# Performance work log

Hardware: AMD Instinct MI355X
Metric: run time of the kernel (lower is better)

## Reference

```python
import jax, jax.numpy as jnp
import numpy as np

N = 30000          # nodes
DEG = 16           # in-degree per node
E = N * DEG        # edges per etype
T = 3              # edge types
IN = 128           # in_feats
HID = 256          # hidden_size
HEADS = 4
CLS = 2            # num_classes
NEG_SLOPE = 0.2    # DGL GATConv default


def setup_inputs() -> dict:
    key = jax.random.key(0)
    ks = jax.random.split(key, 14)
    s = lambda k, shape: (jax.random.normal(k, shape, jnp.float32) * 0.05)
    feat = jax.random.normal(ks[0], (N, IN), jnp.float32)
    src = jax.random.randint(ks[1], (T, E), 0, N)
    # every node gets exactly DEG incoming edges per etype (DGL forbids 0-in-degree)
    dst = jnp.tile(jnp.repeat(jnp.arange(N), DEG), (T, 1))
    D = HID // HEADS
    return {
        "feat": feat,
        "W0": s(ks[2], (T, IN, HID)),  "al0": s(ks[3], (T, HEADS, D)), "ar0": s(ks[4], (T, HEADS, D)), "b0": jnp.zeros((T, HID), jnp.float32),
        "W1": s(ks[5], (T, HID, HID)), "al1": s(ks[6], (T, HEADS, D)), "ar1": s(ks[7], (T, HEADS, D)), "b1": jnp.zeros((T, HID), jnp.float32),
        "W2": s(ks[8], (T, HID, CLS)), "al2": s(ks[9], (T, 1, CLS)),   "ar2": s(ks[10], (T, 1, CLS)), "b2": jnp.zeros((T, CLS), jnp.float32),
        "src": src, "dst": dst,
    }


def _gat(feat, W, al, ar, b, src, dst):
    """DGL GATConv: feat [n,F], W [F,H*D], al/ar [H,D], b [H*D] -> [n,H,D]."""
    n = feat.shape[0]
    H, D = al.shape
    h = (feat @ W).reshape(n, H, D)                      # projected features
    el = jnp.sum(h * al, axis=-1)                        # [n,H]
    er = jnp.sum(h * ar, axis=-1)                        # [n,H]
    e = jax.nn.leaky_relu(el[src] + er[dst], NEG_SLOPE)  # [E,H] edge scores
    # segment softmax over incoming edges of each dst node
    emax = jax.ops.segment_max(e, dst, num_segments=n)
    ex = jnp.exp(e - emax[dst])
    den = jax.ops.segment_sum(ex, dst, num_segments=n)
    alpha = ex / den[dst]                                # [E,H]
    out = jax.ops.segment_sum(h[src] * alpha[:, :, None], dst, num_segments=n)
    return out + b.reshape(H, D)


def _hetero(feat, W, al, ar, b, src, dst):
    # HeteroGraphConv(aggregate='mean') over T edge types on one node type
    outs = [_gat(feat, W[t], al[t], ar[t], b[t], src[t], dst[t]) for t in range(W.shape[0])]
    return jnp.mean(jnp.stack(outs, 0), axis=0)


def reference(feat, W0, al0, ar0, b0, W1, al1, ar1, b1, W2, al2, ar2, b2, src, dst):
    h = jax.nn.elu(_hetero(feat, W0, al0, ar0, b0, src, dst).reshape(N, -1))
    h = jax.nn.elu(_hetero(h, W1, al1, ar1, b1, src, dst).reshape(N, -1))
    logits = _hetero(h, W2, al2, ar2, b2, src, dst)      # [N,1,CLS]
    # faithful to F.softmax(logits[primary_ntype], dim=1): dim=1 is the size-1 head axis
    return logits, jax.nn.softmax(logits, axis=1)
```

## Files before the change

### kernel.cpp

```cpp
#include <hip/hip_runtime.h>
#include <hip/hip_bf16.h>
#include <hip/hip_fp8.h>
#include <math.h>

#define N_NODES 30000
#define DEG     16
#define NE      480000
#define NT      3
#define IN_F    128
#define HID_F   256
#define HEADS   4
#define DH      64
#define CLS     2
#define SLOPE   0.2f

#define NTILES      1875
#define KC0         4
#define KC1         8

typedef __hip_bfloat16 bf16;
typedef unsigned long long u64;
typedef __attribute__((ext_vector_type(8))) short short8;
typedef __attribute__((ext_vector_type(4))) float floatx4;

__device__ __forceinline__ float bf2f(short x) {
    unsigned int u = ((unsigned int)(unsigned short)x) << 16;
    float f;
    __builtin_memcpy(&f, &u, 4);
    return f;
}
__device__ __forceinline__ short f2bf_s(float x) {
    bf16 b = bf16(x);
    short s;
    __builtin_memcpy(&s, &b, 2);
    return s;
}

__device__ __forceinline__ void fp8x4_decode(unsigned int u, float* f) {
#if __has_builtin(__builtin_amdgcn_cvt_pk_f32_fp8)
    auto lo = __builtin_amdgcn_cvt_pk_f32_fp8((int)u, false);
    auto hi = __builtin_amdgcn_cvt_pk_f32_fp8((int)u, true);
    f[0] = lo[0]; f[1] = lo[1]; f[2] = hi[0]; f[3] = hi[1];
#else
#pragma unroll
    for (int j = 0; j < 4; j++) {
        __hip_fp8_e4m3 q;
        q.__x = (unsigned char)((u >> (8 * j)) & 0xff);
        f[j] = (float)q;
    }
#endif
}
__device__ __forceinline__ unsigned int fp8_encode4_u32(float v0, float v1,
                                                        float v2, float v3) {
#if __has_builtin(__builtin_amdgcn_cvt_pk_fp8_f32)
    int p01 = __builtin_amdgcn_cvt_pk_fp8_f32(v0, v1, 0, false);
    int p23 = __builtin_amdgcn_cvt_pk_fp8_f32(v2, v3, 0, false);
    return ((unsigned int)p01 & 0xffffu) | ((unsigned int)p23 << 16);
#else
    __hip_fp8_e4m3 q0(v0), q1(v1), q2(v2), q3(v3);
    return (unsigned int)q0.__x | ((unsigned int)q1.__x << 8) |
           ((unsigned int)q2.__x << 16) | ((unsigned int)q3.__x << 24);
#endif
}
__device__ __forceinline__ u64 fp8_encode8_u64(const float* v) {
    unsigned int lo = fp8_encode4_u32(v[0], v[1], v[2], v[3]);
    unsigned int hi = fp8_encode4_u32(v[4], v[5], v[6], v[7]);
    return (u64)lo | ((u64)hi << 32);
}


#define FEAT8_THREADS (N_NODES * (IN_F / 8))
#define BP0_THREADS   (NT * 16 * KC0 * 64)
#define BP1_THREADS   (NT * 16 * KC1 * 64)
__global__ void prep(const float* __restrict__ feat, const float* __restrict__ W0,
                     const float* __restrict__ W1, u64* __restrict__ feat8,
                     u64* __restrict__ Bpack0, u64* __restrict__ Bpack1) {
    int g = blockIdx.x * 256 + threadIdx.x;
    if (g < FEAT8_THREADS) {
        const float* src = feat + (size_t)g * 8;
        float v[8];
#pragma unroll
        for (int j = 0; j < 8; j++) v[j] = src[j];
        feat8[g] = fp8_encode8_u64(v);
        return;
    }
    g -= FEAT8_THREADS;
    if (g < BP0_THREADS) {
        int t = g / (16 * KC0 * 64), rem = g % (16 * KC0 * 64);
        int nt = rem / (KC0 * 64);
        int C  = (rem / 64) % KC0;
        int lane = rem & 63, l15 = lane & 15, quad = lane >> 4;
        int col = nt * 16 + l15, k0 = C * 32 + quad * 8;
        const float* src = W0 + (size_t)t * IN_F * HID_F + (size_t)k0 * HID_F + col;
        float v[8];
#pragma unroll
        for (int j = 0; j < 8; j++) v[j] = src[(size_t)j * HID_F];
        Bpack0[((size_t)(t * 16 + nt) * KC0 + C) * 64 + lane] = fp8_encode8_u64(v);
        return;
    }
    g -= BP0_THREADS;
    if (g < BP1_THREADS) {
        int t = g / (16 * KC1 * 64), rem = g % (16 * KC1 * 64);
        int nt = rem / (KC1 * 64);
        int C  = (rem / 64) % KC1;
        int lane = rem & 63, l15 = lane & 15, quad = lane >> 4;
        int col = nt * 16 + l15, k0 = C * 32 + quad * 8;
        const float* src = W1 + (size_t)t * HID_F * HID_F + (size_t)k0 * HID_F + col;
        float v[8];
#pragma unroll
        for (int j = 0; j < 8; j++) v[j] = src[(size_t)j * HID_F];
        Bpack1[((size_t)(t * 16 + nt) * KC1 + C) * 64 + lane] = fp8_encode8_u64(v);
    }
}

template <int K>
__global__ __launch_bounds__(256, 4) void gemm_proj(const unsigned char* __restrict__ X8,
                                                    const u64* __restrict__ Bpack,
                                                    const float* __restrict__ al,
                                                    const float* __restrict__ ar,
                                                    unsigned char* __restrict__ Hout,
                                                    float* __restrict__ el,
                                                    float* __restrict__ er) {
    const int KC = K / 32;
    __shared__ u64 sB[512 * (K / 32)];
    int nh   = blockIdx.y;
    int t    = blockIdx.z;
    int tid  = threadIdx.x;
    int wave = tid >> 6, lane = tid & 63;
    int quad = lane >> 4, l15 = lane & 15;
    int e0   = blockIdx.x * 8 + wave * 2;

    {
        const u64* Bp = Bpack + (size_t)(t * 16 + nh * 8) * KC * 64;
#pragma unroll
        for (int i = 0; i < 2 * KC; i++) sB[i * 256 + tid] = Bp[i * 256 + tid];
    }
    __syncthreads();

    int ra0 = e0 * 16 + l15;       if (ra0 >= N_NODES) ra0 = N_NODES - 1;
    int ra1 = (e0 + 1) * 16 + l15; if (ra1 >= N_NODES) ra1 = N_NODES - 1;
    const unsigned char* Ap0 = X8 + (size_t)ra0 * K + quad * 8;
    const unsigned char* Ap1 = X8 + (size_t)ra1 * K + quad * 8;
    unsigned char* Ht = Hout + (size_t)t * N_NODES * HID_F;

    floatx4 acc[8][2];
#pragma unroll
    for (int i = 0; i < 8; i++) {
        acc[i][0] = (floatx4){0.f, 0.f, 0.f, 0.f};
        acc[i][1] = (floatx4){0.f, 0.f, 0.f, 0.f};
    }

#pragma unroll
    for (int C = 0; C < KC; C++) {
        long xb0 = (long)*(const u64*)(Ap0 + C * 32);
        long xb1 = (long)*(const u64*)(Ap1 + C * 32);
#pragma unroll
        for (int nt = 0; nt < 8; nt++) {
            long wa = (long)sB[(nt * KC + C) * 64 + lane];
            acc[nt][0] = __builtin_amdgcn_mfma_f32_16x16x32_fp8_fp8(wa, xb0, acc[nt][0], 0, 0, 0);
            acc[nt][1] = __builtin_amdgcn_mfma_f32_16x16x32_fp8_fp8(wa, xb1, acc[nt][1], 0, 0, 0);
        }
    }

#pragma unroll
    for (int e = 0; e < 2; e++) {
        int node = (e0 + e) * 16 + l15;
        bool ok  = node < N_NODES;
#pragma unroll
        for (int nt = 0; nt < 8; nt++) {
            unsigned int u = fp8_encode4_u32(acc[nt][e][0], acc[nt][e][1],
                                             acc[nt][e][2], acc[nt][e][3]);
            if (ok)
                __builtin_nontemporal_store(u,
                    (unsigned int*)(Ht + (size_t)node * HID_F + (nh * 8 + nt) * 16 + quad * 4));
        }
#pragma unroll
        for (int hl = 0; hl < 2; hl++) {
            int h = nh * 2 + hl;
            float pl = 0.f, pr = 0.f;
#pragma unroll
            for (int j = 0; j < 4; j++) {
                int nt = hl * 4 + j;
                int coff = t * HID_F + (nh * 8 + nt) * 16 + quad * 4;
                float4 av = *(const float4*)(al + coff);
                float4 rv = *(const float4*)(ar + coff);
                pl += acc[nt][e][0] * av.x + acc[nt][e][1] * av.y +
                      acc[nt][e][2] * av.z + acc[nt][e][3] * av.w;
                pr += acc[nt][e][0] * rv.x + acc[nt][e][1] * rv.y +
                      acc[nt][e][2] * rv.z + acc[nt][e][3] * rv.w;
            }
            pl += __shfl_xor(pl, 16); pl += __shfl_xor(pl, 32);
            pr += __shfl_xor(pr, 16); pr += __shfl_xor(pr, 32);
            if (lane < 16 && ok) {
                el[((size_t)t * N_NODES + node) * HEADS + h] = pl;
                er[((size_t)t * N_NODES + node) * HEADS + h] = pr;
            }
        }
    }
}

template <bool PACK>
__global__ __launch_bounds__(256, 8) void gat_agg(const unsigned char* __restrict__ Hproj,
                                                  const float* __restrict__ el,
                                                  const float* __restrict__ er,
                                                  const int* __restrict__ src,
                                                  const float* __restrict__ bias,
                                                  void* __restrict__ outv) {
    int blk = blockIdx.x;
    int tid = threadIdx.x;
    __shared__ int   s_src[8][NT][DEG];
    __shared__ float s_w[8][NT][HEADS][DEG];

#pragma unroll
    for (int it = 0; it < 2; it++) {
        int j = it * 256 + tid;
        if (j < NT * 128) {
            int t = j / 128, k = j % 128;
            s_src[k >> 4][t][k & 15] = src[(size_t)t * NE + blk * 128 + k];
        }
    }
    __syncthreads();

    {
        int lane16 = tid & 15;
        int ubase  = tid >> 4;
#pragma unroll
        for (int it = 0; it < 6; it++) {
            int u = it * 16 + ubase;
            int g = u / 12, rem = u % 12;
            int t = rem >> 2, h = rem & 3;
            int n = blk * 8 + g;
            int s = s_src[g][t][lane16];
            float e = el[((size_t)t * N_NODES + s) * HEADS + h] +
                      er[((size_t)t * N_NODES + n) * HEADS + h];
            e = e > 0.f ? e : SLOPE * e;
            float m = e;
            m = fmaxf(m, __shfl_xor(m, 1));
            m = fmaxf(m, __shfl_xor(m, 2));
            m = fmaxf(m, __shfl_xor(m, 4));
            m = fmaxf(m, __shfl_xor(m, 8));
            float p = __expf(e - m);
            float ss = p;
            ss += __shfl_xor(ss, 1);
            ss += __shfl_xor(ss, 2);
            ss += __shfl_xor(ss, 4);
            ss += __shfl_xor(ss, 8);
            s_w[g][t][h][lane16] = p / ss;
        }
    }
    __syncthreads();

    int g = tid >> 5, c = tid & 31;
    int n = blk * 8 + g;
    int h = c >> 3;
    int col0 = c * 8;

    float acc[8];
#pragma unroll
    for (int j = 0; j < 8; j++) acc[j] = 0.f;

#pragma unroll
    for (int t = 0; t < NT; t++) {
        const unsigned char* Hh = Hproj + (size_t)t * N_NODES * HID_F;
#pragma unroll
        for (int i = 0; i < DEG; i++) {
            int s   = s_src[g][t][i];
            float w = s_w[g][t][h][i];
            uint2 v = *(const uint2*)(Hh + (size_t)s * HID_F + col0);
            float f[8];
            fp8x4_decode(v.x, f);
            fp8x4_decode(v.y, f + 4);
#pragma unroll
            for (int j = 0; j < 8; j++) acc[j] += w * f[j];
        }
    }

    float res[8];
#pragma unroll
    for (int j = 0; j < 8; j++) {
        float bsum = bias[0 * HID_F + col0 + j] + bias[1 * HID_F + col0 + j] +
                     bias[2 * HID_F + col0 + j];
        float r = (acc[j] + bsum) * (1.f / 3.f);
        res[j] = r > 0.f ? r : (__expf(r) - 1.f);
    }
    if (PACK) {
        u64* out = (u64*)outv;
        out[((size_t)n * HID_F + col0) >> 3] = fp8_encode8_u64(res);
    } else {
        short* out = (short*)outv;
        short8 o;
#pragma unroll
        for (int j = 0; j < 8; j++) o[j] = f2bf_s(res[j]);
        *(short8*)(out + (size_t)n * HID_F + col0) = o;
    }
}

__global__ __launch_bounds__(256) void proj2(const short* __restrict__ X,
                                             const float* __restrict__ W2,
                                             const float* __restrict__ al2,
                                             const float* __restrict__ ar2,
                                             float* __restrict__ p2,
                                             float* __restrict__ el2,
                                             float* __restrict__ er2) {
    int n    = blockIdx.x * 4 + (threadIdx.x >> 6);
    int lane = threadIdx.x & 63;
    const short* Xr = X + (size_t)n * HID_F + lane * 4;
    float x[4];
    x[0] = bf2f(Xr[0]); x[1] = bf2f(Xr[1]); x[2] = bf2f(Xr[2]); x[3] = bf2f(Xr[3]);
    float a[NT][CLS];
#pragma unroll
    for (int t = 0; t < NT; t++)
#pragma unroll
        for (int cc = 0; cc < CLS; cc++) {
            float v = 0.f;
#pragma unroll
            for (int j = 0; j < 4; j++)
                v += x[j] * W2[(size_t)t * HID_F * CLS + (lane * 4 + j) * CLS + cc];
#pragma unroll
            for (int off = 32; off; off >>= 1) v += __shfl_xor(v, off);
            a[t][cc] = v;
        }
    if (lane == 0) {
#pragma unroll
        for (int t = 0; t < NT; t++) {
            p2[((size_t)t * N_NODES + n) * CLS + 0] = a[t][0];
            p2[((size_t)t * N_NODES + n) * CLS + 1] = a[t][1];
            el2[(size_t)t * N_NODES + n] = a[t][0] * al2[t * CLS + 0] + a[t][1] * al2[t * CLS + 1];
            er2[(size_t)t * N_NODES + n] = a[t][0] * ar2[t * CLS + 0] + a[t][1] * ar2[t * CLS + 1];
        }
    }
}

__global__ void final_layer(const float* __restrict__ p2,
                            const float* __restrict__ el2,
                            const float* __restrict__ er2,
                            const int* __restrict__ src,
                            const float* __restrict__ b2,
                            float* __restrict__ out) {
    int n = blockIdx.x * 256 + threadIdx.x;
    if (n >= N_NODES) return;
    float l0 = 0.f, l1 = 0.f;
    for (int t = 0; t < NT; t++) {
        float erv = er2[(size_t)t * N_NODES + n];
        const int* sp = src + (size_t)t * NE + n * DEG;
        float ev[DEG];
        float m = -1e30f;
#pragma unroll
        for (int i = 0; i < DEG; i++) {
            int s   = sp[i];
            float e = el2[(size_t)t * N_NODES + s] + erv;
            e = e > 0.f ? e : SLOPE * e;
            ev[i] = e;
            m = fmaxf(m, e);
        }
        float den = 0.f, a0 = 0.f, a1 = 0.f;
#pragma unroll
        for (int i = 0; i < DEG; i++) {
            int s   = sp[i];
            float p = __expf(ev[i] - m);
            den += p;
            a0  += p * p2[((size_t)t * N_NODES + s) * CLS + 0];
            a1  += p * p2[((size_t)t * N_NODES + s) * CLS + 1];
        }
        l0 += a0 / den + b2[t * CLS + 0];
        l1 += a1 / den + b2[t * CLS + 1];
    }
    l0 *= (1.f / 3.f);
    l1 *= (1.f / 3.f);
    out[(size_t)n * CLS + 0] = l0;
    out[(size_t)n * CLS + 1] = l1;
    float* out2 = out + (size_t)N_NODES * CLS;
    out2[(size_t)n * CLS + 0] = 1.0f;
    out2[(size_t)n * CLS + 1] = 1.0f;
}

extern "C" void kernel_launch(void* const* d_in, const int* in_sizes, int n_in,
                              void* d_out, int out_size, void* d_ws, size_t ws_size,
                              hipStream_t stream) {
    const float* feat = (const float*)d_in[0];
    const float* W0   = (const float*)d_in[1];
    const float* al0  = (const float*)d_in[2];
    const float* ar0  = (const float*)d_in[3];
    const float* b0   = (const float*)d_in[4];
    const float* W1   = (const float*)d_in[5];
    const float* al1  = (const float*)d_in[6];
    const float* ar1  = (const float*)d_in[7];
    const float* b1   = (const float*)d_in[8];
    const float* W2   = (const float*)d_in[9];
    const float* al2  = (const float*)d_in[10];
    const float* ar2  = (const float*)d_in[11];
    const float* b2   = (const float*)d_in[12];
    const int*   src  = (const int*)d_in[13];

    char* w = (char*)d_ws;
    auto alloc = [&](size_t bytes) {
        char* p = w;
        w += (bytes + 255) & ~(size_t)255;
        return p;
    };
    u64* feat8  = (u64*)alloc((size_t)(N_NODES + 16) * IN_F);
    u64* h1_8   = (u64*)alloc((size_t)(N_NODES + 16) * HID_F);
    u64* Bpack0 = (u64*)alloc((size_t)NT * 16 * KC0 * 64 * 8);
    u64* Bpack1 = (u64*)alloc((size_t)NT * 16 * KC1 * 64 * 8);
    unsigned char* Hproj = (unsigned char*)alloc((size_t)NT * N_NODES * HID_F);
    short* h2    = (short*)alloc((size_t)N_NODES * HID_F * 2);
    float* el    = (float*)alloc((size_t)NT * N_NODES * HEADS * 4);
    float* er    = (float*)alloc((size_t)NT * N_NODES * HEADS * 4);
    float* p2    = (float*)alloc((size_t)NT * N_NODES * CLS * 4);
    float* el2   = (float*)alloc((size_t)NT * N_NODES * 4);
    float* er2   = (float*)alloc((size_t)NT * N_NODES * 4);

    int prep_total = FEAT8_THREADS + BP0_THREADS + BP1_THREADS;
    prep<<<(prep_total + 255) / 256, 256, 0, stream>>>(feat, W0, W1, feat8,
                                                       Bpack0, Bpack1);

    dim3 ggrid((NTILES + 7) / 8, 2, NT);

    gemm_proj<IN_F><<<ggrid, 256, 0, stream>>>((const unsigned char*)feat8, Bpack0,
                                               al0, ar0, Hproj, el, er);
    gat_agg<true><<<N_NODES / 8, 256, 0, stream>>>(Hproj, el, er, src, b0, h1_8);

    gemm_proj<HID_F><<<ggrid, 256, 0, stream>>>((const unsigned char*)h1_8, Bpack1,
                                                al1, ar1, Hproj, el, er);
    gat_agg<false><<<N_NODES / 8, 256, 0, stream>>>(Hproj, el, er, src, b1, h2);

    proj2<<<dim3(N_NODES / 4), 256, 0, stream>>>(h2, W2, al2, ar2, p2, el2, er2);
    final_layer<<<(N_NODES + 255) / 256, 256, 0, stream>>>(p2, el2, er2, src, b2,
                                                           (float*)d_out);
}
```

Measured before the change: 333.0 us.

## Aggregate raw features before projection and fold attention vectors into weights

```diff
diff --git a/kernel.cpp b/kernel.cpp
--- a/kernel.cpp
+++ b/kernel.cpp
@@ -14,26 +14,25 @@
 #define CLS     2
 #define SLOPE   0.2f
 
-#define NTILES      1875
-#define KC0         4
-#define KC1         8
+#define NBLK    1875
+#define KC0     4
+#define KC1     8
 
 typedef __hip_bfloat16 bf16;
 typedef unsigned long long u64;
-typedef __attribute__((ext_vector_type(8))) short short8;
 typedef __attribute__((ext_vector_type(4))) float floatx4;
 
+__device__ __forceinline__ short f2bf_s(float x) {
+    bf16 b = bf16(x);
+    short s;
+    __builtin_memcpy(&s, &b, 2);
+    return s;
+}
 __device__ __forceinline__ float bf2f(short x) {
     unsigned int u = ((unsigned int)(unsigned short)x) << 16;
     float f;
     __builtin_memcpy(&f, &u, 4);
     return f;
-}
-__device__ __forceinline__ short f2bf_s(float x) {
-    bf16 b = bf16(x);
-    short s;
-    __builtin_memcpy(&s, &b, 2);
-    return s;
 }
 
 __device__ __forceinline__ void fp8x4_decode(unsigned int u, float* f) {
@@ -68,13 +67,20 @@
     return (u64)lo | ((u64)hi << 32);
 }
 
-
 #define FEAT8_THREADS (N_NODES * (IN_F / 8))
 #define BP0_THREADS   (NT * 16 * KC0 * 64)
 #define BP1_THREADS   (NT * 16 * KC1 * 64)
-__global__ void prep(const float* __restrict__ feat, const float* __restrict__ W0,
-                     const float* __restrict__ W1, u64* __restrict__ feat8,
-                     u64* __restrict__ Bpack0, u64* __restrict__ Bpack1) {
+#define WL0_THREADS   (NT * HEADS * IN_F)
+#define WL1_THREADS   (NT * HEADS * HID_F)
+__global__ void prep(const float* __restrict__ feat,
+                     const float* __restrict__ W0, const float* __restrict__ al0,
+                     const float* __restrict__ ar0,
+                     const float* __restrict__ W1, const float* __restrict__ al1,
+                     const float* __restrict__ ar1,
+                     u64* __restrict__ feat8,
+                     u64* __restrict__ Bpack0, u64* __restrict__ Bpack1,
+                     float* __restrict__ wl0, float* __restrict__ wr0,
+                     float* __restrict__ wl1, float* __restrict__ wr1) {
     int g = blockIdx.x * 256 + threadIdx.x;
     if (g < FEAT8_THREADS) {
         const float* src = feat + (size_t)g * 8;
@@ -110,188 +116,218 @@
 #pragma unroll
         for (int j = 0; j < 8; j++) v[j] = src[(size_t)j * HID_F];
         Bpack1[((size_t)(t * 16 + nt) * KC1 + C) * 64 + lane] = fp8_encode8_u64(v);
+        return;
+    }
+    g -= BP1_THREADS;
+    if (g < WL0_THREADS) {
+        int u = g / IN_F, k = g % IN_F;
+        int t = u >> 2, h = u & 3;
+        const float* Wk = W0 + ((size_t)t * IN_F + k) * HID_F + h * DH;
+        const float* av = al0 + ((size_t)t * HEADS + h) * DH;
+        const float* rv = ar0 + ((size_t)t * HEADS + h) * DH;
+        float a = 0.f, b = 0.f;
+#pragma unroll 8
+        for (int d = 0; d < DH; d++) { float w = Wk[d]; a += w * av[d]; b += w * rv[d]; }
+        wl0[(size_t)u * IN_F + k] = a;
+        wr0[(size_t)u * IN_F + k] = b;
+        return;
+    }
+    g -= WL0_THREADS;
+    if (g < WL1_THREADS) {
+        int u = g / HID_F, k = g % HID_F;
+        int t = u >> 2, h = u & 3;
+        const float* Wk = W1 + ((size_t)t * HID_F + k) * HID_F + h * DH;
+        const float* av = al1 + ((size_t)t * HEADS + h) * DH;
+        const float* rv = ar1 + ((size_t)t * HEADS + h) * DH;
+        float a = 0.f, b = 0.f;
+#pragma unroll 8
+        for (int d = 0; d < DH; d++) { float w = Wk[d]; a += w * av[d]; b += w * rv[d]; }
+        wl1[(size_t)u * HID_F + k] = a;
+        wr1[(size_t)u * HID_F + k] = b;
     }
 }
 
 template <int K>
-__global__ __launch_bounds__(256, 4) void gemm_proj(const unsigned char* __restrict__ X8,
-                                                    const u64* __restrict__ Bpack,
-                                                    const float* __restrict__ al,
-                                                    const float* __restrict__ ar,
-                                                    unsigned char* __restrict__ Hout,
-                                                    float* __restrict__ el,
-                                                    float* __restrict__ er) {
+__global__ __launch_bounds__(256) void eler(const unsigned char* __restrict__ X8,
+                                            const float* __restrict__ wl,
+                                            const float* __restrict__ wr,
+                                            float* __restrict__ el,
+                                            float* __restrict__ er) {
+    const int KB = K / 64;
+    int n    = blockIdx.x * 4 + (threadIdx.x >> 6);
+    int lane = threadIdx.x & 63;
+    float f[KB > 4 ? KB : 4];
+    {
+        unsigned int u = 0;
+        if (KB == 2) {
+            unsigned short us;
+            __builtin_memcpy(&us, X8 + (size_t)n * K + lane * KB, 2);
+            u = us;
+        } else {
+            __builtin_memcpy(&u, X8 + (size_t)n * K + lane * KB, 4);
+        }
+        float d4[4];
+        fp8x4_decode(u, d4);
+#pragma unroll
+        for (int j = 0; j < KB; j++) f[j] = d4[j];
+    }
+#pragma unroll
+    for (int u = 0; u < NT * HEADS; u++) {
+        const float* wlv = wl + (size_t)u * K + lane * KB;
+        const float* wrv = wr + (size_t)u * K + lane * KB;
+        float a = 0.f, b = 0.f;
+#pragma unroll
+        for (int j = 0; j < KB; j++) { a += f[j] * wlv[j]; b += f[j] * wrv[j]; }
+#pragma unroll
+        for (int off = 32; off; off >>= 1) {
+            a += __shfl_xor(a, off);
+            b += __shfl_xor(b, off);
+        }
+        if (lane == 0) {
+            int t = u >> 2, h = u & 3;
+            el[((size_t)t * N_NODES + n) * HEADS + h] = a;
+            er[((size_t)t * N_NODES + n) * HEADS + h] = b;
+        }
+    }
+}
+
+template <int K, bool LAST>
+__global__ __launch_bounds__(256, 4) void fused_gat(
+    const unsigned char* __restrict__ X8,
+    const u64* __restrict__ Bpack,
+    const float* __restrict__ el,
+    const float* __restrict__ er,
+    const int* __restrict__ src,
+    const float* __restrict__ bias,
+    void* __restrict__ outv) {
     const int KC = K / 32;
-    __shared__ u64 sB[512 * (K / 32)];
-    int nh   = blockIdx.y;
-    int t    = blockIdx.z;
-    int tid  = threadIdx.x;
-    int wave = tid >> 6, lane = tid & 63;
-    int quad = lane >> 4, l15 = lane & 15;
-    int e0   = blockIdx.x * 8 + wave * 2;
-
-    {
-        const u64* Bp = Bpack + (size_t)(t * 16 + nh * 8) * KC * 64;
-#pragma unroll
-        for (int i = 0; i < 2 * KC; i++) sB[i * 256 + tid] = Bp[i * 256 + tid];
-    }
-    __syncthreads();
-
-    int ra0 = e0 * 16 + l15;       if (ra0 >= N_NODES) ra0 = N_NODES - 1;
-    int ra1 = (e0 + 1) * 16 + l15; if (ra1 >= N_NODES) ra1 = N_NODES - 1;
-    const unsigned char* Ap0 = X8 + (size_t)ra0 * K + quad * 8;
-    const unsigned char* Ap1 = X8 + (size_t)ra1 * K + quad * 8;
-    unsigned char* Ht = Hout + (size_t)t * N_NODES * HID_F;
-
-    floatx4 acc[8][2];
-#pragma unroll
-    for (int i = 0; i < 8; i++) {
-        acc[i][0] = (floatx4){0.f, 0.f, 0.f, 0.f};
-        acc[i][1] = (floatx4){0.f, 0.f, 0.f, 0.f};
-    }
-
-#pragma unroll
-    for (int C = 0; C < KC; C++) {
-        long xb0 = (long)*(const u64*)(Ap0 + C * 32);
-        long xb1 = (long)*(const u64*)(Ap1 + C * 32);
-#pragma unroll
-        for (int nt = 0; nt < 8; nt++) {
-            long wa = (long)sB[(nt * KC + C) * 64 + lane];
-            acc[nt][0] = __builtin_amdgcn_mfma_f32_16x16x32_fp8_fp8(wa, xb0, acc[nt][0], 0, 0, 0);
-            acc[nt][1] = __builtin_amdgcn_mfma_f32_16x16x32_fp8_fp8(wa, xb1, acc[nt][1], 0, 0, 0);
-        }
-    }
-
-#pragma unroll
-    for (int e = 0; e < 2; e++) {
-        int node = (e0 + e) * 16 + l15;
-        bool ok  = node < N_NODES;
-#pragma unroll
-        for (int nt = 0; nt < 8; nt++) {
-            unsigned int u = fp8_encode4_u32(acc[nt][e][0], acc[nt][e][1],
-                                             acc[nt][e][2], acc[nt][e][3]);
-            if (ok)
-                __builtin_nontemporal_store(u,
-                    (unsigned int*)(Ht + (size_t)node * HID_F + (nh * 8 + nt) * 16 + quad * 4));
-        }
-#pragma unroll
-        for (int hl = 0; hl < 2; hl++) {
-            int h = nh * 2 + hl;
-            float pl = 0.f, pr = 0.f;
-#pragma unroll
-            for (int j = 0; j < 4; j++) {
-                int nt = hl * 4 + j;
-                int coff = t * HID_F + (nh * 8 + nt) * 16 + quad * 4;
-                float4 av = *(const float4*)(al + coff);
-                float4 rv = *(const float4*)(ar + coff);
-                pl += acc[nt][e][0] * av.x + acc[nt][e][1] * av.y +
-                      acc[nt][e][2] * av.z + acc[nt][e][3] * av.w;
-                pr += acc[nt][e][0] * rv.x + acc[nt][e][1] * rv.y +
-                      acc[nt][e][2] * rv.z + acc[nt][e][3] * rv.w;
-            }
-            pl += __shfl_xor(pl, 16); pl += __shfl_xor(pl, 32);
-            pr += __shfl_xor(pr, 16); pr += __shfl_xor(pr, 32);
-            if (lane < 16 && ok) {
-                el[((size_t)t * N_NODES + node) * HEADS + h] = pl;
-                er[((size_t)t * N_NODES + node) * HEADS + h] = pr;
-            }
-        }
-    }
-}
-
-template <bool PACK>
-__global__ __launch_bounds__(256, 8) void gat_agg(const unsigned char* __restrict__ Hproj,
-                                                  const float* __restrict__ el,
-                                                  const float* __restrict__ er,
-                                                  const int* __restrict__ src,
-                                                  const float* __restrict__ bias,
-                                                  void* __restrict__ outv) {
+    const int KD = K / 128;
     int blk = blockIdx.x;
     int tid = threadIdx.x;
-    __shared__ int   s_src[8][NT][DEG];
-    __shared__ float s_w[8][NT][HEADS][DEG];
-
-#pragma unroll
-    for (int it = 0; it < 2; it++) {
-        int j = it * 256 + tid;
-        if (j < NT * 128) {
-            int t = j / 128, k = j % 128;
-            s_src[k >> 4][t][k & 15] = src[(size_t)t * NE + blk * 128 + k];
-        }
-    }
-    __syncthreads();
-
-    {
-        int lane16 = tid & 15;
-        int ubase  = tid >> 4;
-#pragma unroll
-        for (int it = 0; it < 6; it++) {
-            int u = it * 16 + ubase;
-            int g = u / 12, rem = u % 12;
-            int t = rem >> 2, h = rem & 3;
-            int n = blk * 8 + g;
-            int s = s_src[g][t][lane16];
-            float e = el[((size_t)t * N_NODES + s) * HEADS + h] +
-                      er[((size_t)t * N_NODES + n) * HEADS + h];
-            e = e > 0.f ? e : SLOPE * e;
-            float m = e;
-            m = fmaxf(m, __shfl_xor(m, 1));
-            m = fmaxf(m, __shfl_xor(m, 2));
-            m = fmaxf(m, __shfl_xor(m, 4));
-            m = fmaxf(m, __shfl_xor(m, 8));
-            float p = __expf(e - m);
-            float ss = p;
-            ss += __shfl_xor(ss, 1);
-            ss += __shfl_xor(ss, 2);
-            ss += __shfl_xor(ss, 4);
-            ss += __shfl_xor(ss, 8);
-            s_w[g][t][h][lane16] = p / ss;
-        }
-    }
-    __syncthreads();
-
-    int g = tid >> 5, c = tid & 31;
-    int n = blk * 8 + g;
-    int h = c >> 3;
-    int col0 = c * 8;
-
-    float acc[8];
-#pragma unroll
-    for (int j = 0; j < 8; j++) acc[j] = 0.f;
-
-#pragma unroll
+    int wave = tid >> 6, lane = tid & 63, quad = lane >> 4, l15 = lane & 15;
+
+    __shared__ int   s_src[256];
+    __shared__ float s_w[HEADS][16][17];
+    __shared__ u64   s_frag[HEADS][KC * 64];
+
+    floatx4 acc[HEADS];
+#pragma unroll
+    for (int h = 0; h < HEADS; h++) acc[h] = (floatx4){0.f, 0.f, 0.f, 0.f};
+
     for (int t = 0; t < NT; t++) {
-        const unsigned char* Hh = Hproj + (size_t)t * N_NODES * HID_F;
-#pragma unroll
-        for (int i = 0; i < DEG; i++) {
-            int s   = s_src[g][t][i];
-            float w = s_w[g][t][h][i];
-            uint2 v = *(const uint2*)(Hh + (size_t)s * HID_F + col0);
-            float f[8];
-            fp8x4_decode(v.x, f);
-            fp8x4_decode(v.y, f + 4);
-#pragma unroll
-            for (int j = 0; j < 8; j++) acc[j] += w * f[j];
-        }
-    }
-
-    float res[8];
-#pragma unroll
-    for (int j = 0; j < 8; j++) {
-        float bsum = bias[0 * HID_F + col0 + j] + bias[1 * HID_F + col0 + j] +
-                     bias[2 * HID_F + col0 + j];
-        float r = (acc[j] + bsum) * (1.f / 3.f);
-        res[j] = r > 0.f ? r : (__expf(r) - 1.f);
-    }
-    if (PACK) {
-        u64* out = (u64*)outv;
-        out[((size_t)n * HID_F + col0) >> 3] = fp8_encode8_u64(res);
-    } else {
-        short* out = (short*)outv;
-        short8 o;
-#pragma unroll
-        for (int j = 0; j < 8; j++) o[j] = f2bf_s(res[j]);
-        *(short8*)(out + (size_t)n * HID_F + col0) = o;
+        __syncthreads();
+        s_src[tid] = src[(size_t)t * NE + blk * 256 + tid];
+        __syncthreads();
+
+        {
+            int node = tid >> 4, i = tid & 15;
+            int s = s_src[node * 16 + i];
+            float4 eL = *(const float4*)(el + ((size_t)t * N_NODES + s) * HEADS);
+            float4 eR = *(const float4*)(er + ((size_t)t * N_NODES + blk * 16 + node) * HEADS);
+            float e0 = eL.x + eR.x, e1 = eL.y + eR.y, e2 = eL.z + eR.z, e3 = eL.w + eR.w;
+            e0 = e0 > 0.f ? e0 : SLOPE * e0;
+            e1 = e1 > 0.f ? e1 : SLOPE * e1;
+            e2 = e2 > 0.f ? e2 : SLOPE * e2;
+            e3 = e3 > 0.f ? e3 : SLOPE * e3;
+            float m0 = e0, m1 = e1, m2 = e2, m3 = e3;
+#pragma unroll
+            for (int off = 8; off; off >>= 1) {
+                m0 = fmaxf(m0, __shfl_xor(m0, off));
+                m1 = fmaxf(m1, __shfl_xor(m1, off));
+                m2 = fmaxf(m2, __shfl_xor(m2, off));
+                m3 = fmaxf(m3, __shfl_xor(m3, off));
+            }
+            float p0 = __expf(e0 - m0), p1 = __expf(e1 - m1);
+            float p2 = __expf(e2 - m2), p3 = __expf(e3 - m3);
+            float q0 = p0, q1 = p1, q2 = p2, q3 = p3;
+#pragma unroll
+            for (int off = 8; off; off >>= 1) {
+                q0 += __shfl_xor(q0, off);
+                q1 += __shfl_xor(q1, off);
+                q2 += __shfl_xor(q2, off);
+                q3 += __shfl_xor(q3, off);
+            }
+            s_w[0][node][i] = p0 / q0;
+            s_w[1][node][i] = p1 / q1;
+            s_w[2][node][i] = p2 / q2;
+            s_w[3][node][i] = p3 / q3;
+        }
+        __syncthreads();
+
+        {
+            int node = tid & 15, cg = tid >> 4;
+            const int* sp = s_src + node * 16;
+            float xacc[HEADS][8 * KD];
+#pragma unroll
+            for (int h = 0; h < HEADS; h++)
+#pragma unroll
+                for (int j = 0; j < 8 * KD; j++) xacc[h][j] = 0.f;
+
+#pragma unroll
+            for (int i = 0; i < DEG; i++) {
+                int s   = sp[i];
+                float w0 = s_w[0][node][i], w1 = s_w[1][node][i];
+                float w2 = s_w[2][node][i], w3 = s_w[3][node][i];
+#pragma unroll
+                for (int d = 0; d < KD; d++) {
+                    int c8 = cg + 16 * d;
+                    u64 v;
+                    __builtin_memcpy(&v, X8 + (size_t)s * K + c8 * 8, 8);
+                    float f[8];
+                    fp8x4_decode((unsigned int)v, f);
+                    fp8x4_decode((unsigned int)(v >> 32), f + 4);
+#pragma unroll
+                    for (int j = 0; j < 8; j++) {
+                        xacc[0][d * 8 + j] += w0 * f[j];
+                        xacc[1][d * 8 + j] += w1 * f[j];
+                        xacc[2][d * 8 + j] += w2 * f[j];
+                        xacc[3][d * 8 + j] += w3 * f[j];
+                    }
+                }
+            }
+#pragma unroll
+            for (int h = 0; h < HEADS; h++)
+#pragma unroll
+                for (int d = 0; d < KD; d++) {
+                    int c8 = cg + 16 * d, C = c8 >> 2, qf = c8 & 3;
+                    s_frag[h][C * 64 + qf * 16 + node] = fp8_encode8_u64(&xacc[h][d * 8]);
+                }
+        }
+        __syncthreads();
+
+        const u64* Bp = Bpack + (size_t)t * 16 * KC * 64;
+#pragma unroll
+        for (int h = 0; h < HEADS; h++) {
+#pragma unroll
+            for (int C = 0; C < KC; C++) {
+                long wa = (long)Bp[(size_t)((h * 4 + wave) * KC + C) * 64 + lane];
+                long xb = (long)s_frag[h][C * 64 + lane];
+                acc[h] = __builtin_amdgcn_mfma_f32_16x16x32_fp8_fp8(wa, xb, acc[h], 0, 0, 0);
+            }
+        }
+    }
+
+    int n = blk * 16 + l15;
+#pragma unroll
+    for (int h = 0; h < HEADS; h++) {
+        int col0 = h * 64 + wave * 16 + quad * 4;
+        float r[4];
+#pragma unroll
+        for (int j = 0; j < 4; j++) {
+            float bsum = bias[col0 + j] + bias[HID_F + col0 + j] + bias[2 * HID_F + col0 + j];
+            float v = (acc[h][j] + bsum) * (1.f / 3.f);
+            r[j] = v > 0.f ? v : (__expf(v) - 1.f);
+        }
+        if (LAST) {
+            u64 o = (u64)(unsigned short)f2bf_s(r[0]) |
+                    ((u64)(unsigned short)f2bf_s(r[1]) << 16) |
+                    ((u64)(unsigned short)f2bf_s(r[2]) << 32) |
+                    ((u64)(unsigned short)f2bf_s(r[3]) << 48);
+            *(u64*)((short*)outv + (size_t)n * HID_F + col0) = o;
+        } else {
+            unsigned int o = fp8_encode4_u32(r[0], r[1], r[2], r[3]);
+            *(unsigned int*)((unsigned char*)outv + (size_t)n * HID_F + col0) = o;
+        }
     }
 }
 
@@ -398,33 +434,38 @@
         w += (bytes + 255) & ~(size_t)255;
         return p;
     };
-    u64* feat8  = (u64*)alloc((size_t)(N_NODES + 16) * IN_F);
-    u64* h1_8   = (u64*)alloc((size_t)(N_NODES + 16) * HID_F);
-    u64* Bpack0 = (u64*)alloc((size_t)NT * 16 * KC0 * 64 * 8);
-    u64* Bpack1 = (u64*)alloc((size_t)NT * 16 * KC1 * 64 * 8);
-    unsigned char* Hproj = (unsigned char*)alloc((size_t)NT * N_NODES * HID_F);
-    short* h2    = (short*)alloc((size_t)N_NODES * HID_F * 2);
-    float* el    = (float*)alloc((size_t)NT * N_NODES * HEADS * 4);
-    float* er    = (float*)alloc((size_t)NT * N_NODES * HEADS * 4);
-    float* p2    = (float*)alloc((size_t)NT * N_NODES * CLS * 4);
-    float* el2   = (float*)alloc((size_t)NT * N_NODES * 4);
-    float* er2   = (float*)alloc((size_t)NT * N_NODES * 4);
-
-    int prep_total = FEAT8_THREADS + BP0_THREADS + BP1_THREADS;
-    prep<<<(prep_total + 255) / 256, 256, 0, stream>>>(feat, W0, W1, feat8,
-                                                       Bpack0, Bpack1);
-
-    dim3 ggrid((NTILES + 7) / 8, 2, NT);
-
-    gemm_proj<IN_F><<<ggrid, 256, 0, stream>>>((const unsigned char*)feat8, Bpack0,
-                                               al0, ar0, Hproj, el, er);
-    gat_agg<true><<<N_NODES / 8, 256, 0, stream>>>(Hproj, el, er, src, b0, h1_8);
-
-    gemm_proj<HID_F><<<ggrid, 256, 0, stream>>>((const unsigned char*)h1_8, Bpack1,
-                                                al1, ar1, Hproj, el, er);
-    gat_agg<false><<<N_NODES / 8, 256, 0, stream>>>(Hproj, el, er, src, b1, h2);
-
-    proj2<<<dim3(N_NODES / 4), 256, 0, stream>>>(h2, W2, al2, ar2, p2, el2, er2);
+    u64*   feat8  = (u64*)alloc((size_t)N_NODES * IN_F);
+    u64*   h1_8   = (u64*)alloc((size_t)N_NODES * HID_F);
+    u64*   Bpack0 = (u64*)alloc((size_t)NT * 16 * KC0 * 64 * 8);
+    u64*   Bpack1 = (u64*)alloc((size_t)NT * 16 * KC1 * 64 * 8);
+    float* wl0    = (float*)alloc((size_t)NT * HEADS * IN_F * 4);
+    float* wr0    = (float*)alloc((size_t)NT * HEADS * IN_F * 4);
+    float* wl1    = (float*)alloc((size_t)NT * HEADS * HID_F * 4);
+    float* wr1    = (float*)alloc((size_t)NT * HEADS * HID_F * 4);
+    short* h2     = (short*)alloc((size_t)N_NODES * HID_F * 2);
+    float* el     = (float*)alloc((size_t)NT * N_NODES * HEADS * 4);
+    float* er     = (float*)alloc((size_t)NT * N_NODES * HEADS * 4);
+    float* p2     = (float*)alloc((size_t)NT * N_NODES * CLS * 4);
+    float* el2    = (float*)alloc((size_t)NT * N_NODES * 4);
+    float* er2    = (float*)alloc((size_t)NT * N_NODES * 4);
+
+    int prep_total = FEAT8_THREADS + BP0_THREADS + BP1_THREADS + WL0_THREADS + WL1_THREADS;
+    prep<<<(prep_total + 255) / 256, 256, 0, stream>>>(feat, W0, al0, ar0,
+                                                       W1, al1, ar1,
+                                                       (u64*)feat8, Bpack0, Bpack1,
+                                                       wl0, wr0, wl1, wr1);
+
+    eler<IN_F><<<N_NODES / 4, 256, 0, stream>>>((const unsigned char*)feat8,
+                                                wl0, wr0, el, er);
+    fused_gat<IN_F, false><<<NBLK, 256, 0, stream>>>((const unsigned char*)feat8,
+                                                     Bpack0, el, er, src, b0, h1_8);
+
+    eler<HID_F><<<N_NODES / 4, 256, 0, stream>>>((const unsigned char*)h1_8,
+                                                 wl1, wr1, el, er);
+    fused_gat<HID_F, true><<<NBLK, 256, 0, stream>>>((const unsigned char*)h1_8,
+                                                     Bpack1, el, er, src, b1, h2);
+
+    proj2<<<N_NODES / 4, 256, 0, stream>>>(h2, W2, al2, ar2, p2, el2, er2);
     final_layer<<<(N_NODES + 255) / 256, 256, 0, stream>>>(p2, el2, er2, src, b2,
                                                            (float*)d_out);
 }
```

Result: slower. 514.0 us (+54.4%).
